# Kernel tuning notes

Measured on AMD Instinct MI355X. Metric: run time of the kernel, lower is better.

The kernel has to match this reference:

```python
import jax, jax.numpy as jnp
import numpy as np

N_HEADS = 12


def setup_inputs() -> dict:
    key = jax.random.key(0)
    k1, k2, k3 = jax.random.split(key, 3)
    B, W, C = 2, 2048, 768
    in_sequence_bwc = jax.random.normal(k1, (B, W, C), dtype=jnp.float32)
    # QKV projection weight [3C, C] (torch Linear convention: out_features x in_features)
    w_attn = jax.random.normal(k2, (3 * C, C), dtype=jnp.float32) * (1.0 / np.sqrt(C))
    w_proj = jax.random.normal(k3, (C, C), dtype=jnp.float32) * (1.0 / np.sqrt(C))
    return {"in_sequence_bwc": in_sequence_bwc, "w_attn": w_attn, "w_proj": w_proj}


def reference(in_sequence_bwc, w_attn, w_proj):
    B, W, C = in_sequence_bwc.shape
    H = N_HEADS
    K = C // H  # head dim
    qkv = jnp.einsum('bwc,dc->bwd', in_sequence_bwc, w_attn)  # [B,W,3C]
    q, k, v = jnp.split(qkv, 3, axis=-1)
    # [B,H,W,K]
    q = q.reshape(B, W, H, K).transpose(0, 2, 1, 3)
    k = k.reshape(B, W, H, K).transpose(0, 2, 1, 3)
    v = v.reshape(B, W, H, K).transpose(0, 2, 1, 3)
    scores = jnp.einsum('bhqk,bhsk->bhqs', q, k) / jnp.sqrt(jnp.float32(K))
    causal = jnp.tril(jnp.ones((W, W), dtype=bool))
    scores = jnp.where(causal[None, None], scores, jnp.float32(-jnp.inf))
    probs = jax.nn.softmax(scores, axis=-1)
    out = jnp.einsum('bhqs,bhsk->bhqk', probs, v)  # [B,H,W,K]
    out = out.transpose(0, 2, 1, 3).reshape(B, W, C)
    return jnp.einsum('bwc,dc->bwd', out, w_proj)
```

## Files before the change

kernel.cpp:

```cpp
#include <hip/hip_runtime.h>

constexpr int B_  = 2;
constexpr int W_  = 2048;
constexpr int C_  = 768;
constexpr int H_  = 12;
constexpr int HD  = 64;
constexpr int C3  = 3 * C_;
constexpr int M_  = B_ * W_;
constexpr int NSLOT = 80;

typedef float  f32x4 __attribute__((ext_vector_type(4)));
typedef short  s16x8 __attribute__((ext_vector_type(8)));
typedef short  s16x4 __attribute__((ext_vector_type(4)));
typedef unsigned short u16;
typedef unsigned int   u32;

__device__ __forceinline__ u16 f2bf(float f) {
    unsigned int u = __float_as_uint(f);
    u += 0x7FFFu + ((u >> 16) & 1u);
    return (u16)(u >> 16);
}

__device__ __forceinline__ void gload_lds16(const u16* g, u16* l) {
    __builtin_amdgcn_global_load_lds(
        (const __attribute__((address_space(1))) unsigned int*)g,
        (__attribute__((address_space(3))) unsigned int*)l, 16, 0, 0);
}

__global__ __launch_bounds__(256)
void cvt_all(const float* __restrict__ x, const float* __restrict__ wa,
             const float* __restrict__ wp, u16* __restrict__ xb,
             u16* __restrict__ wab, u16* __restrict__ wpb)
{
    const int n0 = M_ * C_ / 8;
    const int n1 = n0 + C3 * C_ / 8;
    const int n2 = n1 + C_ * C_ / 8;
    int i = blockIdx.x * 256 + threadIdx.x;
    const float* s; u16* d; int j;
    if (i < n0)      { s = x;  d = xb;  j = i; }
    else if (i < n1) { s = wa; d = wab; j = i - n0; }
    else if (i < n2) { s = wp; d = wpb; j = i - n1; }
    else return;
    const float4 a = reinterpret_cast<const float4*>(s)[j * 2];
    const float4 b = reinterpret_cast<const float4*>(s)[j * 2 + 1];
    s16x8 v;
    v[0] = (short)f2bf(a.x); v[1] = (short)f2bf(a.y);
    v[2] = (short)f2bf(a.z); v[3] = (short)f2bf(a.w);
    v[4] = (short)f2bf(b.x); v[5] = (short)f2bf(b.y);
    v[6] = (short)f2bf(b.z); v[7] = (short)f2bf(b.w);
    reinterpret_cast<s16x8*>(d)[j] = v;
}

__device__ __forceinline__ void store_out(u16*  p, float v) { *p = f2bf(v); }
__device__ __forceinline__ void store_out(float* p, float v) { *p = v; }

template <typename OutT>
__global__ __launch_bounds__(256)
void gemm_nt_mfma(const u16* __restrict__ A, const u16* __restrict__ Bm,
                  OutT* __restrict__ Y, int Ndim, int Kdim)
{
    __shared__ __align__(16) u16 As[128 * 64];
    __shared__ __align__(16) u16 Bs[128 * 64];

    const int t  = threadIdx.x;
    const int w  = t >> 6;
    const int l  = t & 63;
    const int lg = l >> 4;
    const int ln = l & 15;
    const int wm = w >> 1;
    const int wn = w & 1;
    const int m0 = blockIdx.x * 128;
    const int n0 = blockIdx.y * 128;

    f32x4 acc[4][4];
    #pragma unroll
    for (int mi = 0; mi < 4; ++mi)
        #pragma unroll
        for (int ni = 0; ni < 4; ++ni)
            acc[mi][ni] = (f32x4){0.f, 0.f, 0.f, 0.f};

    for (int k0 = 0; k0 < Kdim; k0 += 64) {
        #pragma unroll
        for (int it = 0; it < 4; ++it) {
            const int c  = t + it * 256;
            const int fr = c >> 7;
            const int s  = (c >> 6) & 1;
            const int kc = (c >> 4) & 3;
            const int rr = c & 15;
            const size_t koff = (size_t)k0 + s * 32 + kc * 8;
            const u16* ga = A  + (size_t)(m0 + fr * 16 + rr) * Kdim + koff;
            const u16* gb = Bm + (size_t)(n0 + fr * 16 + rr) * Kdim + koff;
            gload_lds16(ga, &As[(size_t)(it * 256 + w * 64) * 8]);
            gload_lds16(gb, &Bs[(size_t)(it * 256 + w * 64) * 8]);
        }
        __syncthreads();

        #pragma unroll
        for (int s = 0; s < 2; ++s) {
            s16x8 af[4], bf[4];
            #pragma unroll
            for (int mi = 0; mi < 4; ++mi)
                af[mi] = *reinterpret_cast<const s16x8*>(
                    &As[(size_t)((wm * 4 + mi) * 128 + s * 64 + lg * 16 + ln) * 8]);
            #pragma unroll
            for (int ni = 0; ni < 4; ++ni)
                bf[ni] = *reinterpret_cast<const s16x8*>(
                    &Bs[(size_t)((wn * 4 + ni) * 128 + s * 64 + lg * 16 + ln) * 8]);
            __builtin_amdgcn_s_setprio(1);
            #pragma unroll
            for (int mi = 0; mi < 4; ++mi)
                #pragma unroll
                for (int ni = 0; ni < 4; ++ni)
                    acc[mi][ni] = __builtin_amdgcn_mfma_f32_16x16x32_bf16(
                        af[mi], bf[ni], acc[mi][ni], 0, 0, 0);
            __builtin_amdgcn_s_setprio(0);
        }
        __syncthreads();
    }

    #pragma unroll
    for (int mi = 0; mi < 4; ++mi) {
        const int row = m0 + wm * 64 + mi * 16 + lg * 4;
        #pragma unroll
        for (int ni = 0; ni < 4; ++ni) {
            const int col = n0 + wn * 64 + ni * 16 + ln;
            #pragma unroll
            for (int r = 0; r < 4; ++r)
                store_out(&Y[(size_t)(row + r) * Ndim + col], acc[mi][ni][r]);
        }
    }
}

__global__ __launch_bounds__(256)
void attn_partial(const u16* __restrict__ qkv, float* __restrict__ po,
                  float* __restrict__ pl)
{
    __shared__ __align__(16) unsigned char KsB[64 * 128];
    __shared__ __align__(16) unsigned char VtB[64 * 144];
    __shared__ __align__(16) unsigned char OnesB[16 * 144];

    const int t  = threadIdx.x;
    const int w  = t >> 6;
    const int l  = t & 63;
    const int lg = l >> 4;
    const int ln = l & 15;
    const int p  = blockIdx.x;
    const int h  = blockIdx.y;
    const int b  = blockIdx.z;

    if (t < 576) ((u32*)OnesB)[t] = (t < 36) ? 0x3F803F80u : 0u;

    int qt, ck;
    if (p < 8)       { qt = p;                 ck = 0; }
    else if (p < 24) { qt = 8  + ((p - 8) >> 1);  ck = (p - 8) & 1; }
    else if (p < 48) { qt = 16 + (p - 24) / 3;    ck = (p - 24) % 3; }
    else             { qt = 24 + ((p - 48) >> 2); ck = (p - 48) & 3; }

    const int qb  = qt * 64;
    const int q0w = qb + w * 16;
    const int g0  = ck * 8;
    const int g1  = min(qt + 1, g0 + 8);
    const int slot = (b * H_ + h) * NSLOT + p;

    const u16* base  = qkv + (size_t)(b * W_) * C3;
    const u16* kbase = base + C_ + h * HD;
    const u16* vbase = base + 2 * C_ + h * HD;

    s16x8 qf[2];
    {
        const u16* qrow = base + (size_t)(q0w + ln) * C3 + h * HD;
        #pragma unroll
        for (int kc = 0; kc < 2; ++kc)
            qf[kc] = *reinterpret_cast<const s16x8*>(&qrow[kc * 32 + lg * 8]);
    }

    f32x4 o[4];
    #pragma unroll
    for (int i = 0; i < 4; ++i) o[i] = (f32x4){0.f, 0.f, 0.f, 0.f};
    f32x4 o4 = (f32x4){0.f, 0.f, 0.f, 0.f};

    const float c1 = 0.18033688011112042f;
    const float c2 = 17.312340490667562f;

    const int sk_key0 = t >> 3;
    const int sk_d8   = (t & 7) * 8;
    const int sv_kq   = t >> 4;
    const int sv_d4   = (t & 15) * 4;
    const int sv_pos  = ((sv_kq >> 3) << 5) + ((sv_kq & 3) << 3)
                      + (((sv_kq >> 2) & 1) << 2);

    s16x8 kr[2];
    s16x4 vr[4];

    {
        const int s0 = g0 * 64;
        kr[0] = *reinterpret_cast<const s16x8*>(
            &kbase[(size_t)(s0 + sk_key0) * C3 + sk_d8]);
        kr[1] = *reinterpret_cast<const s16x8*>(
            &kbase[(size_t)(s0 + sk_key0 + 32) * C3 + sk_d8]);
        const u16* vsrc = vbase + (size_t)(s0 + sv_kq * 4) * C3 + sv_d4;
        #pragma unroll
        for (int j = 0; j < 4; ++j)
            vr[j] = *reinterpret_cast<const s16x4*>(&vsrc[(size_t)j * C3]);
    }

    for (int g = g0; g < g1; ++g) {
        const int s0 = g * 64;

        __syncthreads();

        #pragma unroll
        for (int it = 0; it < 2; ++it) {
            const int key = sk_key0 + it * 32;
            int woff = key * 128 + sk_d8 * 2;
            woff ^= (key & 7) << 4;
            *reinterpret_cast<s16x8*>(KsB + woff) = kr[it];
        }
        #pragma unroll
        for (int j = 0; j < 4; ++j) {
            s16x4 pk = { vr[0][j], vr[1][j], vr[2][j], vr[3][j] };
            *reinterpret_cast<s16x4*>(VtB + (sv_d4 + j) * 144 + sv_pos * 2) = pk;
        }

        if (g + 1 < g1) {
            const int s1 = s0 + 64;
            kr[0] = *reinterpret_cast<const s16x8*>(
                &kbase[(size_t)(s1 + sk_key0) * C3 + sk_d8]);
            kr[1] = *reinterpret_cast<const s16x8*>(
                &kbase[(size_t)(s1 + sk_key0 + 32) * C3 + sk_d8]);
            const u16* vsrc = vbase + (size_t)(s1 + sv_kq * 4) * C3 + sv_d4;
            #pragma unroll
            for (int j = 0; j < 4; ++j)
                vr[j] = *reinterpret_cast<const s16x4*>(&vsrc[(size_t)j * C3]);
        }

        __syncthreads();

        #pragma unroll
        for (int c = 0; c < 2; ++c) {
            if (s0 + c * 32 <= q0w + 15) {
                float pt[2][4];
                #pragma unroll
                for (int n2 = 0; n2 < 2; ++n2) {
                    const int krow = c * 32 + n2 * 16 + ln;
                    f32x4 s = (f32x4){0.f, 0.f, 0.f, 0.f};
                    s16x8 kf0, kf1;
                    {
                        int r0 = krow * 128 + lg * 16;       r0 ^= (krow & 7) << 4;
                        int r1 = krow * 128 + 64 + lg * 16;  r1 ^= (krow & 7) << 4;
                        kf0 = *reinterpret_cast<const s16x8*>(KsB + r0);
                        kf1 = *reinterpret_cast<const s16x8*>(KsB + r1);
                    }
                    __builtin_amdgcn_s_setprio(1);
                    s = __builtin_amdgcn_mfma_f32_16x16x32_bf16(kf0, qf[0], s, 0, 0, 0);
                    s = __builtin_amdgcn_mfma_f32_16x16x32_bf16(kf1, qf[1], s, 0, 0, 0);
                    __builtin_amdgcn_s_setprio(0);
                    const int kg0  = s0 + c * 32 + n2 * 16 + lg * 4;
                    const int klast = s0 + c * 32 + n2 * 16 + 15;
                    if (klast <= q0w) {
                        #pragma unroll
                        for (int r = 0; r < 4; ++r)
                            pt[n2][r] = exp2f(fmaf(s[r], c1, -c2));
                    } else {
                        const int qg = q0w + ln;
                        #pragma unroll
                        for (int r = 0; r < 4; ++r)
                            pt[n2][r] = (kg0 + r <= qg)
                                      ? exp2f(fmaf(s[r], c1, -c2)) : 0.0f;
                    }
                }
                union { s16x8 v; u32 wd[4]; } afu;
                asm("v_cvt_pk_bf16_f32 %0, %1, %2"
                    : "=v"(afu.wd[0]) : "v"(pt[0][0]), "v"(pt[0][1]));
                asm("v_cvt_pk_bf16_f32 %0, %1, %2"
                    : "=v"(afu.wd[1]) : "v"(pt[0][2]), "v"(pt[0][3]));
                asm("v_cvt_pk_bf16_f32 %0, %1, %2"
                    : "=v"(afu.wd[2]) : "v"(pt[1][0]), "v"(pt[1][1]));
                asm("v_cvt_pk_bf16_f32 %0, %1, %2"
                    : "=v"(afu.wd[3]) : "v"(pt[1][2]), "v"(pt[1][3]));
                const s16x8 af = afu.v;
                s16x8 vf[4];
                #pragma unroll
                for (int dt = 0; dt < 4; ++dt)
                    vf[dt] = *reinterpret_cast<const s16x8*>(
                        VtB + (dt * 16 + ln) * 144 + c * 64 + lg * 16);
                s16x8 vf4 = *reinterpret_cast<const s16x8*>(
                    OnesB + ln * 144 + c * 64 + lg * 16);
                __builtin_amdgcn_s_setprio(1);
                #pragma unroll
                for (int dt = 0; dt < 4; ++dt)
                    o[dt] = __builtin_amdgcn_mfma_f32_16x16x32_bf16(af, vf[dt], o[dt], 0, 0, 0);
                o4 = __builtin_amdgcn_mfma_f32_16x16x32_bf16(af, vf4, o4, 0, 0, 0);
                __builtin_amdgcn_s_setprio(0);
            }
        }
    }

    if (ln == 0) {
        #pragma unroll
        for (int r = 0; r < 4; ++r)
            pl[(size_t)slot * 64 + w * 16 + lg * 4 + r] = o4[r];
    }
    float* os = po + (size_t)slot * 4096;
    #pragma unroll
    for (int r = 0; r < 4; ++r)
        #pragma unroll
        for (int dt = 0; dt < 4; ++dt)
            os[(w * 16 + lg * 4 + r) * 64 + dt * 16 + ln] = o[dt][r];
}

__global__ __launch_bounds__(256)
void attn_combine(const float* __restrict__ po, const float* __restrict__ pl,
                  u16* __restrict__ aob)
{
    const int qt = blockIdx.x;
    const int h  = blockIdx.y;
    const int b  = blockIdx.z;
    const int nc = (qt + 8) >> 3;
    int cum;
    if (qt < 8)       cum = qt;
    else if (qt < 16) cum = 8  + 2 * (qt - 8);
    else if (qt < 24) cum = 24 + 3 * (qt - 16);
    else              cum = 48 + 4 * (qt - 24);
    const int slot0 = (b * H_ + h) * NSLOT + cum;

    const int tid = threadIdx.x;
    const int i   = tid >> 2;
    const int d0  = (tid & 3) * 16;

    f32x4 acc[4] = { (f32x4){0,0,0,0}, (f32x4){0,0,0,0},
                     (f32x4){0,0,0,0}, (f32x4){0,0,0,0} };
    float lt = 0.0f;
    for (int c = 0; c < nc; ++c) {
        const float* os = po + (size_t)(slot0 + c) * 4096 + i * 64 + d0;
        #pragma unroll
        for (int v = 0; v < 4; ++v)
            acc[v] += *reinterpret_cast<const f32x4*>(os + v * 4);
        lt += pl[(size_t)(slot0 + c) * 64 + i];
    }
    const float inv = 1.0f / lt;

    u16* dst = aob + (size_t)(b * W_ + qt * 64 + i) * C_ + h * HD + d0;
    s16x8 ov[2];
    #pragma unroll
    for (int v = 0; v < 4; ++v)
        #pragma unroll
        for (int e = 0; e < 4; ++e)
            ov[v >> 1][(v & 1) * 4 + e] = (short)f2bf(acc[v][e] * inv);
    *reinterpret_cast<s16x8*>(dst)     = ov[0];
    *reinterpret_cast<s16x8*>(dst + 8) = ov[1];
}

extern "C" void kernel_launch(void* const* d_in, const int* in_sizes, int n_in,
                              void* d_out, int out_size, void* d_ws, size_t ws_size,
                              hipStream_t stream)
{
    const float* x      = (const float*)d_in[0];
    const float* w_attn = (const float*)d_in[1];
    const float* w_proj = (const float*)d_in[2];
    float* out = (float*)d_out;

    u16* xb   = (u16*)d_ws;
    u16* wab  = xb   + (size_t)M_ * C_;
    u16* wpb  = wab  + (size_t)C3 * C_;
    u16* qkvb = wpb  + (size_t)C_ * C_;
    u16* aob  = qkvb + (size_t)M_ * C3;
    float* po = (float*)(aob + (size_t)M_ * C_);
    float* pl = po + (size_t)B_ * H_ * NSLOT * 4096;

    {
        const int total8 = (M_ * C_ + C3 * C_ + C_ * C_) / 8;
        cvt_all<<<(total8 + 255) / 256, 256, 0, stream>>>(
            x, w_attn, w_proj, xb, wab, wpb);
    }

    {
        dim3 grid(M_ / 128, C3 / 128);
        gemm_nt_mfma<u16><<<grid, 256, 0, stream>>>(xb, wab, qkvb, C3, C_);
    }

    {
        dim3 grid(NSLOT, H_, B_);
        attn_partial<<<grid, 256, 0, stream>>>(qkvb, po, pl);
    }
    {
        dim3 grid(W_ / 64, H_, B_);
        attn_combine<<<grid, 256, 0, stream>>>(po, pl, aob);
    }

    {
        dim3 grid(M_ / 128, C_ / 128);
        gemm_nt_mfma<float><<<grid, 256, 0, stream>>>(aob, wpb, out, C_, C_);
    }
}
```

Baseline: 130.4 us.

## Read K fragments from global, double-buffer V in LDS, compute row sums on VALU

The attention partial kernel no longer stages K in shared memory. Each lane loads its MFMA K fragments directly from global memory, which relies on L2 and cache hits. The transposed V tile is now double-buffered so the next tile is written after compute, leaving one barrier per iteration instead of two. The softmax denominator moves from an extra MFMA against a ones matrix to a per-lane fp32 sum reduced with cross-lane shuffles, and launch bounds now request higher occupancy. The trade-off is extra global-load latency on the QK path and possible register pressure from the occupancy hint.

```diff
diff --git a/kernel.cpp b/kernel.cpp
--- a/kernel.cpp
+++ b/kernel.cpp
@@ -131,13 +131,11 @@
     }
 }
 
-__global__ __launch_bounds__(256)
+__global__ __launch_bounds__(256, 8)
 void attn_partial(const u16* __restrict__ qkv, float* __restrict__ po,
                   float* __restrict__ pl)
 {
-    __shared__ __align__(16) unsigned char KsB[64 * 128];
-    __shared__ __align__(16) unsigned char VtB[64 * 144];
-    __shared__ __align__(16) unsigned char OnesB[16 * 144];
+    __shared__ __align__(16) unsigned char VtB[2][64 * 144];
 
     const int t  = threadIdx.x;
     const int w  = t >> 6;
@@ -148,8 +146,6 @@
     const int h  = blockIdx.y;
     const int b  = blockIdx.z;
 
-    if (t < 576) ((u32*)OnesB)[t] = (t < 36) ? 0x3F803F80u : 0u;
-
     int qt, ck;
     if (p < 8)       { qt = p;                 ck = 0; }
     else if (p < 24) { qt = 8  + ((p - 8) >> 1);  ck = (p - 8) & 1; }
@@ -174,67 +170,51 @@
             qf[kc] = *reinterpret_cast<const s16x8*>(&qrow[kc * 32 + lg * 8]);
     }
 
+    const u16* kln = kbase + (size_t)ln * C3 + lg * 8;
+
     f32x4 o[4];
     #pragma unroll
     for (int i = 0; i < 4; ++i) o[i] = (f32x4){0.f, 0.f, 0.f, 0.f};
-    f32x4 o4 = (f32x4){0.f, 0.f, 0.f, 0.f};
+    float lsum = 0.0f;
 
     const float c1 = 0.18033688011112042f;
     const float c2 = 17.312340490667562f;
 
-    const int sk_key0 = t >> 3;
-    const int sk_d8   = (t & 7) * 8;
-    const int sv_kq   = t >> 4;
-    const int sv_d4   = (t & 15) * 4;
-    const int sv_pos  = ((sv_kq >> 3) << 5) + ((sv_kq & 3) << 3)
-                      + (((sv_kq >> 2) & 1) << 2);
-
-    s16x8 kr[2];
+    const int sv_kq  = t >> 4;
+    const int sv_d4  = (t & 15) * 4;
+    const int sv_pos = ((sv_kq >> 3) << 5) + ((sv_kq & 3) << 3)
+                     + (((sv_kq >> 2) & 1) << 2);
+
     s16x4 vr[4];
 
     {
-        const int s0 = g0 * 64;
-        kr[0] = *reinterpret_cast<const s16x8*>(
-            &kbase[(size_t)(s0 + sk_key0) * C3 + sk_d8]);
-        kr[1] = *reinterpret_cast<const s16x8*>(
-            &kbase[(size_t)(s0 + sk_key0 + 32) * C3 + sk_d8]);
-        const u16* vsrc = vbase + (size_t)(s0 + sv_kq * 4) * C3 + sv_d4;
+        const u16* vsrc = vbase + (size_t)(g0 * 64 + sv_kq * 4) * C3 + sv_d4;
         #pragma unroll
         for (int j = 0; j < 4; ++j)
             vr[j] = *reinterpret_cast<const s16x4*>(&vsrc[(size_t)j * C3]);
-    }
-
+        #pragma unroll
+        for (int j = 0; j < 4; ++j) {
+            s16x4 pk = { vr[0][j], vr[1][j], vr[2][j], vr[3][j] };
+            *reinterpret_cast<s16x4*>(VtB[0] + (sv_d4 + j) * 144 + sv_pos * 2) = pk;
+        }
+    }
+
+    int cur = 0;
     for (int g = g0; g < g1; ++g) {
         const int s0 = g * 64;
+        const bool pf = (g + 1 < g1);
 
         __syncthreads();
 
-        #pragma unroll
-        for (int it = 0; it < 2; ++it) {
-            const int key = sk_key0 + it * 32;
-            int woff = key * 128 + sk_d8 * 2;
-            woff ^= (key & 7) << 4;
-            *reinterpret_cast<s16x8*>(KsB + woff) = kr[it];
-        }
-        #pragma unroll
-        for (int j = 0; j < 4; ++j) {
-            s16x4 pk = { vr[0][j], vr[1][j], vr[2][j], vr[3][j] };
-            *reinterpret_cast<s16x4*>(VtB + (sv_d4 + j) * 144 + sv_pos * 2) = pk;
-        }
-
-        if (g + 1 < g1) {
-            const int s1 = s0 + 64;
-            kr[0] = *reinterpret_cast<const s16x8*>(
-                &kbase[(size_t)(s1 + sk_key0) * C3 + sk_d8]);
-            kr[1] = *reinterpret_cast<const s16x8*>(
-                &kbase[(size_t)(s1 + sk_key0 + 32) * C3 + sk_d8]);
-            const u16* vsrc = vbase + (size_t)(s1 + sv_kq * 4) * C3 + sv_d4;
+        if (pf) {
+            const u16* vsrc = vbase + (size_t)(s0 + 64 + sv_kq * 4) * C3 + sv_d4;
             #pragma unroll
             for (int j = 0; j < 4; ++j)
                 vr[j] = *reinterpret_cast<const s16x4*>(&vsrc[(size_t)j * C3]);
         }
 
-        __syncthreads();
+        const u16* kp = kln + (size_t)s0 * C3;
+        const unsigned char* Vc = VtB[cur];
 
         #pragma unroll
         for (int c = 0; c < 2; ++c) {
@@ -242,20 +222,15 @@
                 float pt[2][4];
                 #pragma unroll
                 for (int n2 = 0; n2 < 2; ++n2) {
-                    const int krow = c * 32 + n2 * 16 + ln;
+                    const u16* kpS = kp + (size_t)(c * 32 + n2 * 16) * C3;
+                    s16x8 kf0 = *reinterpret_cast<const s16x8*>(kpS);
+                    s16x8 kf1 = *reinterpret_cast<const s16x8*>(kpS + 32);
                     f32x4 s = (f32x4){0.f, 0.f, 0.f, 0.f};
-                    s16x8 kf0, kf1;
-                    {
-                        int r0 = krow * 128 + lg * 16;       r0 ^= (krow & 7) << 4;
-                        int r1 = krow * 128 + 64 + lg * 16;  r1 ^= (krow & 7) << 4;
-                        kf0 = *reinterpret_cast<const s16x8*>(KsB + r0);
-                        kf1 = *reinterpret_cast<const s16x8*>(KsB + r1);
-                    }
                     __builtin_amdgcn_s_setprio(1);
                     s = __builtin_amdgcn_mfma_f32_16x16x32_bf16(kf0, qf[0], s, 0, 0, 0);
                     s = __builtin_amdgcn_mfma_f32_16x16x32_bf16(kf1, qf[1], s, 0, 0, 0);
                     __builtin_amdgcn_s_setprio(0);
-                    const int kg0  = s0 + c * 32 + n2 * 16 + lg * 4;
+                    const int kg0   = s0 + c * 32 + n2 * 16 + lg * 4;
                     const int klast = s0 + c * 32 + n2 * 16 + 15;
                     if (klast <= q0w) {
                         #pragma unroll
@@ -269,6 +244,9 @@
                                       ? exp2f(fmaf(s[r], c1, -c2)) : 0.0f;
                     }
                 }
+                #pragma unroll
+                for (int r = 0; r < 4; ++r)
+                    lsum += pt[0][r] + pt[1][r];
                 union { s16x8 v; u32 wd[4]; } afu;
                 asm("v_cvt_pk_bf16_f32 %0, %1, %2"
                     : "=v"(afu.wd[0]) : "v"(pt[0][0]), "v"(pt[0][1]));
@@ -283,23 +261,31 @@
                 #pragma unroll
                 for (int dt = 0; dt < 4; ++dt)
                     vf[dt] = *reinterpret_cast<const s16x8*>(
-                        VtB + (dt * 16 + ln) * 144 + c * 64 + lg * 16);
-                s16x8 vf4 = *reinterpret_cast<const s16x8*>(
-                    OnesB + ln * 144 + c * 64 + lg * 16);
+                        Vc + (dt * 16 + ln) * 144 + c * 64 + lg * 16);
                 __builtin_amdgcn_s_setprio(1);
                 #pragma unroll
                 for (int dt = 0; dt < 4; ++dt)
                     o[dt] = __builtin_amdgcn_mfma_f32_16x16x32_bf16(af, vf[dt], o[dt], 0, 0, 0);
-                o4 = __builtin_amdgcn_mfma_f32_16x16x32_bf16(af, vf4, o4, 0, 0, 0);
                 __builtin_amdgcn_s_setprio(0);
             }
         }
-    }
-
-    if (ln == 0) {
-        #pragma unroll
-        for (int r = 0; r < 4; ++r)
-            pl[(size_t)slot * 64 + w * 16 + lg * 4 + r] = o4[r];
+
+        if (pf) {
+            #pragma unroll
+            for (int j = 0; j < 4; ++j) {
+                s16x4 pk = { vr[0][j], vr[1][j], vr[2][j], vr[3][j] };
+                *reinterpret_cast<s16x4*>(
+                    VtB[cur ^ 1] + (sv_d4 + j) * 144 + sv_pos * 2) = pk;
+            }
+        }
+        cur ^= 1;
+    }
+
+    {
+        float v = lsum;
+        v += __shfl_xor(v, 16);
+        v += __shfl_xor(v, 32);
+        if (lg == 0) pl[(size_t)slot * 64 + w * 16 + ln] = v;
     }
     float* os = po + (size_t)slot * 4096;
     #pragma unroll
```

Result: slower. 224.8 us (+72.4%).
